# Kernel optimization log

Measured on AMD Instinct MI355X. Metric: run time of the kernel, lower is better.

The kernel has to match this reference:

```python
import jax, jax.numpy as jnp
import numpy as np
import math

EMBED_DIM = 256
NUM_HEADS = 8
FFN_DIM = 1024
EPS = 1e-5


def layer_norm(x, g, b):
    mu = jnp.mean(x, axis=-1, keepdims=True)
    var = jnp.var(x, axis=-1, keepdims=True)
    return (x - mu) / jnp.sqrt(var + EPS) * g + b


def setup_inputs() -> dict:
    key = jax.random.key(0)
    ks = jax.random.split(key, 10)
    B, L, D, F = 4, 2048, EMBED_DIM, FFN_DIM
    x = jax.random.normal(ks[0], (B, L, D), dtype=jnp.float32)
    mask = jnp.ones((B, L), dtype=jnp.int32)
    # FFN params (PyTorch Linear default-ish scale)
    W1 = jax.random.normal(ks[1], (D, F), dtype=jnp.float32) / np.sqrt(D)
    b1 = jnp.zeros((F,), dtype=jnp.float32)
    W2 = jax.random.normal(ks[2], (F, D), dtype=jnp.float32) / np.sqrt(F)
    b2 = jnp.zeros((D,), dtype=jnp.float32)
    g1 = jnp.ones((D,), dtype=jnp.float32)
    be1 = jnp.zeros((D,), dtype=jnp.float32)
    g2 = jnp.ones((D,), dtype=jnp.float32)
    be2 = jnp.zeros((D,), dtype=jnp.float32)
    return {"x": x, "mask": mask, "W1": W1, "b1": b1, "W2": W2, "b2": b2,
            "g1": g1, "be1": be1, "g2": g2, "be2": be2}


def quantum_attention(x, mask):
    B, L, D = x.shape
    H, dk = NUM_HEADS, D // NUM_HEADS
    xh = x.reshape(B, L, H, dk).transpose(0, 2, 1, 3)  # [B,H,L,dk]
    # per-token mean over batch and heads -> [L, dk]
    m = jnp.mean(xh, axis=(0, 1))
    # closed form of the single-qubit RX circuit: P(|1>) = sin^2(angle/2)
    dot = m @ m.T  # [L, L]
    ang = jnp.clip(dot, -math.pi, math.pi)
    scores = jnp.sin(ang * 0.5) ** 2  # [L, L], shared across B and H
    attn = jnp.broadcast_to(scores[None, None], (B, H, L, L))
    attn = jnp.where(mask[:, None, None, :] == 0, -1e9, attn)
    attn = jax.nn.softmax(attn, axis=-1)
    out = jnp.einsum('bhij,bhjd->bhid', attn, xh)  # values are xh itself
    return out.transpose(0, 2, 1, 3).reshape(B, L, D)


def reference(x, mask, W1, b1, W2, b2, g1, be1, g2, be2):
    attn_out = quantum_attention(x, mask)
    h = layer_norm(x + attn_out, g1, be1)
    ffn = jax.nn.relu(h @ W1 + b1) @ W2 + b2
    return layer_norm(h + ffn, g2, be2)
```

## Files before the change

### kernel.cpp

```cpp
#include <hip/hip_runtime.h>
#include <hip/hip_bf16.h>


#define B_ 4
#define L_ 2048
#define D_ 256
#define F_ 1024
#define PI_F 3.14159265358979323846f

typedef __bf16 bf16x8 __attribute__((ext_vector_type(8)));
typedef float floatx4 __attribute__((ext_vector_type(4)));
typedef unsigned short ushortx4 __attribute__((ext_vector_type(4)));
typedef unsigned short ushortx8 __attribute__((ext_vector_type(8)));

#define WAIT_VM(n) asm volatile("s_waitcnt vmcnt(" #n ")" ::: "memory")
#define WAIT_LGKM() asm volatile("s_waitcnt lgkmcnt(0)" ::: "memory")
#define SCHED0() __builtin_amdgcn_sched_barrier(0)
#define BARRIER() do { SCHED0(); __builtin_amdgcn_s_barrier(); SCHED0(); } while (0)

__device__ __forceinline__ unsigned short f2bf(float f) {
    unsigned int u = __float_as_uint(f);
    u = (u + 0x7FFFu + ((u >> 16) & 1u)) >> 16;
    return (unsigned short)u;
}
__device__ __forceinline__ float bf2f(unsigned short u) {
    union { unsigned int i; float f; } v; v.i = ((unsigned int)u) << 16; return v.f;
}

__device__ __forceinline__ void async_cp16(unsigned short* lds, const unsigned short* g) {
    __builtin_amdgcn_global_load_lds(
        (const __attribute__((address_space(1))) unsigned int*)g,
        (__attribute__((address_space(3))) unsigned int*)lds, 16, 0, 0);
}

__global__ __launch_bounds__(256) void k_prep(const float* __restrict__ x,
                                              const float* __restrict__ W1,
                                              const float* __restrict__ W2,
                                              const int* __restrict__ mask,
                                              unsigned short* __restrict__ mb,
                                              unsigned short* __restrict__ XmT,
                                              unsigned short* __restrict__ W1T,
                                              unsigned short* __restrict__ W2T) {
    __shared__ float tile[32][33];
    int r = blockIdx.x, t = threadIdx.x;
    if (r >= 2560) {
        if (r < 2816) {
            int idx = (r - 2560) * 256 + t;
            int l = idx >> 5, k = idx & 31;
            float s = 0.f;
#pragma unroll
            for (int b = 0; b < B_; b++) {
                const float* xp = x + ((size_t)(b * L_ + l)) * D_ + k;
#pragma unroll
                for (int h = 0; h < 8; h++) s += xp[h * 32];
            }
            mb[idx] = f2bf(s * (1.f / 32.f));
        } else {
#pragma unroll
            for (int c = 0; c < 32; c++) {
                int e = c * 256 + t;
                int b = e >> 11, j = e & (L_ - 1);
                XmT[(size_t)(1024 + b) * L_ + j] = mask[b * L_ + j] ? 0x3F80 : 0;
            }
        }
        return;
    }
    const float* in; unsigned short* outp; int R, C; const int* mrow = nullptr; size_t bo = 0;
    int bx, by;
    if (r < 2048) {
        int z = r >> 9, rem = r & 511; by = rem >> 3; bx = rem & 7;
        in = x; outp = XmT; R = L_; C = 256; bo = (size_t)z * R * C; mrow = mask + z * L_;
    } else if (r < 2304) {
        int rem = r - 2048; bx = rem & 31; by = rem >> 5;
        in = W1; outp = W1T; R = 256; C = 1024;
    } else {
        int rem = r - 2304; bx = rem & 7; by = rem >> 3;
        in = W2; outp = W2T; R = 1024; C = 256;
    }
    int r0 = by * 32, c0 = bx * 32;
    int tx = t & 31, ty = t >> 5;
#pragma unroll
    for (int rr = 0; rr < 4; rr++) {
        int rw = ty + rr * 8;
        tile[rw][tx] = in[bo + (size_t)(r0 + rw) * C + c0 + tx];
    }
    float mfac = 1.f;
    if (mrow) mfac = mrow[r0 + tx] ? 1.f : 0.f;
    __syncthreads();
#pragma unroll
    for (int rr = 0; rr < 4; rr++) {
        int c = ty + rr * 8;
        outp[bo + (size_t)(c0 + c) * R + r0 + tx] = f2bf(tile[tx][c] * mfac);
    }
}

__global__ __launch_bounds__(256) void k_scores_mfma(const unsigned short* __restrict__ mb,
                                                     unsigned short* __restrict__ E) {
    const int t = threadIdx.x, lane = t & 63, wid = t >> 6;
    const int wm = (wid >> 1) * 64, wn = (wid & 1) * 32;
    const int lr = lane & 15, lq = lane >> 4;
    int m0 = blockIdx.y * 128, n0 = blockIdx.x * 64;
    bf16x8 af[4], bfr[2];
#pragma unroll
    for (int i = 0; i < 4; i++)
        af[i] = *(const bf16x8*)(mb + (size_t)(m0 + wm + i * 16 + lr) * 32 + lq * 8);
#pragma unroll
    for (int j = 0; j < 2; j++)
        bfr[j] = *(const bf16x8*)(mb + (size_t)(n0 + wn + j * 16 + lr) * 32 + lq * 8);
    floatx4 acc[4][2];
#pragma unroll
    for (int i = 0; i < 4; i++)
#pragma unroll
        for (int j = 0; j < 2; j++) {
            acc[i][j] = (floatx4){0.f, 0.f, 0.f, 0.f};
            acc[i][j] = __builtin_amdgcn_mfma_f32_16x16x32_bf16(af[i], bfr[j], acc[i][j], 0, 0, 0);
        }
#pragma unroll
    for (int i = 0; i < 4; i++)
#pragma unroll
        for (int j = 0; j < 2; j++)
#pragma unroll
            for (int r = 0; r < 4; r++) {
                int row = m0 + wm + i * 16 + lq * 4 + r;
                int col = n0 + wn + j * 16 + lr;
                float d = fminf(fmaxf(acc[i][j][r], -PI_F), PI_F);
                float sn = __sinf(0.5f * d);
                E[(size_t)row * L_ + col] = f2bf(__expf(sn * sn));
            }
}

__global__ __launch_bounds__(256) void k_av(const unsigned short* __restrict__ E,
                                            const unsigned short* __restrict__ XmT,
                                            unsigned short* __restrict__ Cb) {
    __shared__ __align__(16) unsigned short sbuf[3][128 * 64 + 64 * 64];
    const int t = threadIdx.x, lane = t & 63, wid = t >> 6;
    const int wm = (wid >> 1) * 64, wn = (wid & 1) * 32;
    const int lr = lane & 15, lq = lane >> 4;
    const int lrow = lane >> 3, lseg = lane & 7;

    int bid = blockIdx.x;
    int swz = (bid & 7) * 34 + (bid >> 3);
    int m0 = (swz / 17) * 128, n0 = (swz % 17) * 64;

    const unsigned short* Ag[4]; int sAoff[4];
#pragma unroll
    for (int q = 0; q < 4; q++) {
        int rl = wid * 32 + q * 8 + lrow;
        Ag[q] = E + (size_t)(m0 + rl) * L_ + ((lseg - rl) & 7) * 8;
        sAoff[q] = (wid * 32 + q * 8) * 64;
    }
    const unsigned short* Bg[2]; int sBoff[2];
#pragma unroll
    for (int q = 0; q < 2; q++) {
        int rl = wid * 16 + q * 8 + lrow;
        Bg[q] = XmT + (size_t)(n0 + rl) * L_ + ((lseg - rl) & 7) * 8;
        sBoff[q] = 8192 + (wid * 16 + q * 8) * 64;
    }
    int arot[4], aroff[4], brot[2], broff[2];
#pragma unroll
    for (int i = 0; i < 4; i++) { int ar = wm + i * 16 + lr; aroff[i] = ar * 64; arot[i] = lq + ar; }
#pragma unroll
    for (int j = 0; j < 2; j++) { int br = wn + j * 16 + lr; broff[j] = 8192 + br * 64; brot[j] = lq + br; }

    floatx4 acc[4][2];
#pragma unroll
    for (int i = 0; i < 4; i++)
#pragma unroll
        for (int j = 0; j < 2; j++) acc[i][j] = (floatx4){0.f, 0.f, 0.f, 0.f};

    auto stage = [&](unsigned short* base, int k0) {
#pragma unroll
        for (int q = 0; q < 4; q++) async_cp16(base + sAoff[q], Ag[q] + k0);
#pragma unroll
        for (int q = 0; q < 2; q++) async_cp16(base + sBoff[q], Bg[q] + k0);
    };
    auto compute = [&](const unsigned short* base) {
#pragma unroll
        for (int s = 0; s < 2; s++) {
            bf16x8 af[4], bfr[2];
#pragma unroll
            for (int i = 0; i < 4; i++)
                af[i] = *(const bf16x8*)(base + aroff[i] + ((s * 4 + arot[i]) & 7) * 8);
#pragma unroll
            for (int j = 0; j < 2; j++)
                bfr[j] = *(const bf16x8*)(base + broff[j] + ((s * 4 + brot[j]) & 7) * 8);
#pragma unroll
            for (int i = 0; i < 4; i++)
#pragma unroll
                for (int j = 0; j < 2; j++)
                    acc[i][j] = __builtin_amdgcn_mfma_f32_16x16x32_bf16(af[i], bfr[j], acc[i][j], 0, 0, 0);
        }
    };

    unsigned short *p0 = sbuf[0], *p1 = sbuf[1], *p2 = sbuf[2];
    stage(p0, 0); stage(p1, 64); stage(p2, 128);
    WAIT_VM(12); BARRIER();
    for (int p = 0; p < 29; ++p) {
        compute(p0);
        BARRIER();
        stage(p0, (p + 3) << 6);
        WAIT_VM(12); BARRIER();
        unsigned short* tmp = p0; p0 = p1; p1 = p2; p2 = tmp;
    }
    compute(p0);
    BARRIER();
    WAIT_VM(6); BARRIER();
    compute(p1);
    BARRIER();
    WAIT_VM(0); BARRIER();
    compute(p2);

#pragma unroll
    for (int i = 0; i < 4; i++)
#pragma unroll
        for (int j = 0; j < 2; j++)
#pragma unroll
            for (int r = 0; r < 4; r++) {
                int row = m0 + wm + i * 16 + lq * 4 + r;
                int col = n0 + wn + j * 16 + lr;
                Cb[(size_t)row * 1088 + col] = f2bf(acc[i][j][r]);
            }
}

__global__ __launch_bounds__(256, 1) void k_ffn(const float* __restrict__ x,
                                                const unsigned short* __restrict__ Cb,
                                                const unsigned short* __restrict__ W1T,
                                                const unsigned short* __restrict__ W2T,
                                                const float* __restrict__ b1,
                                                const float* __restrict__ b2,
                                                const float* __restrict__ g1, const float* __restrict__ be1,
                                                const float* __restrict__ g2, const float* __restrict__ be2,
                                                float* __restrict__ out) {
    __shared__ __align__(16) unsigned short hA[4 * 32 * 64];
    __shared__ __align__(16) unsigned short W1b[2][4 * 64 * 64];
    __shared__ __align__(16) unsigned short W2b[4 * 64 * 64];
    __shared__ __align__(16) unsigned short t1c[32 * 72];
    __shared__ float red[4][32][2];

    const int t = threadIdx.x, lane = t & 63, wid = t >> 6;
    const int lr = lane & 15, lq = lane >> 4;
    const int half = lane >> 5, l32 = lane & 31;
    const int m0 = blockIdx.x * 32;

    float b1v[16];
#pragma unroll
    for (int c = 0; c < 16; c++) b1v[c] = b1[c * 64 + wid * 16 + lr];
    float4 g1a = *(const float4*)(g1 + l32 * 8);
    float4 g1b = *(const float4*)(g1 + l32 * 8 + 4);
    float4 be1a = *(const float4*)(be1 + l32 * 8);
    float4 be1b = *(const float4*)(be1 + l32 * 8 + 4);
    WAIT_VM(0);

    auto stageW1 = [&](unsigned short* buf, int fc) {
#pragma unroll
        for (int q = 0; q < 8; q++) {
            int kc = q >> 1, sub = q & 1;
            int fl = sub * 32 + wid * 8 + (lane >> 3);
            int kk = lane & 7;
            const unsigned short* src = W1T + (size_t)(fc * 64 + fl) * 256 + kc * 64 + (((kk - fl) & 7) * 8);
            async_cp16(W1b[0] + (buf - W1b[0]) + kc * 4096 + sub * 2048 + wid * 512, src);
        }
    };
    auto stageW2 = [&](int fc) {
#pragma unroll
        for (int q = 0; q < 8; q++) {
            int nc = q >> 1, sub = q & 1;
            int nl = sub * 32 + wid * 8 + (lane >> 3);
            int kk = lane & 7;
            const unsigned short* src = W2T + (size_t)(nc * 64 + nl) * 1024 + fc * 64 + (((kk - nl) & 7) * 8);
            async_cp16(W2b + nc * 4096 + sub * 2048 + wid * 512, src);
        }
    };
    stageW1(W1b[0], 0);
    stageW2(0);
    stageW1(W1b[1], 1);

#pragma unroll
    for (int it = 0; it < 4; it++) {
        int tloc = wid * 8 + it * 2 + half;
        int tok = m0 + tloc;
        int bi = tok >> 11, ii = tok & (L_ - 1);
        float rs = bf2f(Cb[(size_t)ii * 1088 + 1024 + bi]);
        float4 xv0 = *(const float4*)(x + (size_t)tok * D_ + l32 * 8);
        float4 xv1 = *(const float4*)(x + (size_t)tok * D_ + l32 * 8 + 4);
        ushortx8 cv = *(const ushortx8*)(Cb + (size_t)ii * 1088 + bi * 256 + l32 * 8);
        float v[8];
        v[0] = xv0.x + bf2f(cv[0]) / rs; v[1] = xv0.y + bf2f(cv[1]) / rs;
        v[2] = xv0.z + bf2f(cv[2]) / rs; v[3] = xv0.w + bf2f(cv[3]) / rs;
        v[4] = xv1.x + bf2f(cv[4]) / rs; v[5] = xv1.y + bf2f(cv[5]) / rs;
        v[6] = xv1.z + bf2f(cv[6]) / rs; v[7] = xv1.w + bf2f(cv[7]) / rs;
        float s = 0.f, s2 = 0.f;
#pragma unroll
        for (int k = 0; k < 8; k++) { s += v[k]; s2 += v[k] * v[k]; }
#pragma unroll
        for (int o = 1; o < 32; o <<= 1) { s += __shfl_xor(s, o); s2 += __shfl_xor(s2, o); }
        float mu = s * (1.f / 256.f);
        float var = s2 * (1.f / 256.f) - mu * mu;
        float rq = rsqrtf(var + 1e-5f);
        union { bf16x8 v8; unsigned short u[8]; } hv;
        hv.u[0] = f2bf((v[0] - mu) * rq * g1a.x + be1a.x);
        hv.u[1] = f2bf((v[1] - mu) * rq * g1a.y + be1a.y);
        hv.u[2] = f2bf((v[2] - mu) * rq * g1a.z + be1a.z);
        hv.u[3] = f2bf((v[3] - mu) * rq * g1a.w + be1a.w);
        hv.u[4] = f2bf((v[4] - mu) * rq * g1b.x + be1b.x);
        hv.u[5] = f2bf((v[5] - mu) * rq * g1b.y + be1b.y);
        hv.u[6] = f2bf((v[6] - mu) * rq * g1b.z + be1b.z);
        hv.u[7] = f2bf((v[7] - mu) * rq * g1b.w + be1b.w);
        *(bf16x8*)(hA + (l32 >> 3) * 2048 + tloc * 64 + ((((l32 & 7) + tloc) & 7) * 8)) = hv.v8;
    }
    WAIT_LGKM(); BARRIER();

    bf16x8 haf[2][8];
#pragma unroll
    for (int i = 0; i < 2; i++)
#pragma unroll
        for (int kc = 0; kc < 4; kc++)
#pragma unroll
            for (int s = 0; s < 2; s++) {
                int row = i * 16 + lr;
                haf[i][kc * 2 + s] = *(const bf16x8*)(hA + kc * 2048 + row * 64 + (((s * 4 + lq + row) & 7) * 8));
            }

    floatx4 acc[2][4];
#pragma unroll
    for (int i = 0; i < 2; i++)
#pragma unroll
        for (int j = 0; j < 4; j++) acc[i][j] = (floatx4){0.f, 0.f, 0.f, 0.f};

    const int wcol = wid * 16 + lr;
    auto gemm1 = [&](const unsigned short* wb, floatx4 a1[2]) {
#pragma unroll
        for (int kc = 0; kc < 4; kc++)
#pragma unroll
            for (int s = 0; s < 2; s++) {
                bf16x8 bfr = *(const bf16x8*)(wb + kc * 4096 + wcol * 64 + (((s * 4 + lq + wcol) & 7) * 8));
                a1[0] = __builtin_amdgcn_mfma_f32_16x16x32_bf16(haf[0][kc * 2 + s], bfr, a1[0], 0, 0, 0);
                a1[1] = __builtin_amdgcn_mfma_f32_16x16x32_bf16(haf[1][kc * 2 + s], bfr, a1[1], 0, 0, 0);
            }
    };
    auto t1write = [&](floatx4 a1[2], float bv) {
#pragma unroll
        for (int i = 0; i < 2; i++)
#pragma unroll
            for (int r = 0; r < 4; r++)
                t1c[(i * 16 + lq * 4 + r) * 72 + wcol] = f2bf(fmaxf(a1[i][r] + bv, 0.f));
    };
    auto gemm2 = [&]() {
#pragma unroll
        for (int s = 0; s < 2; s++) {
            bf16x8 af0 = *(const bf16x8*)(t1c + lr * 72 + s * 32 + lq * 8);
            bf16x8 af1 = *(const bf16x8*)(t1c + (16 + lr) * 72 + s * 32 + lq * 8);
#pragma unroll
            for (int j = 0; j < 4; j++) {
                int nl = j * 16 + lr;
                bf16x8 bfr = *(const bf16x8*)(W2b + wid * 4096 + nl * 64 + (((s * 4 + lq + nl) & 7) * 8));
                acc[0][j] = __builtin_amdgcn_mfma_f32_16x16x32_bf16(af0, bfr, acc[0][j], 0, 0, 0);
                acc[1][j] = __builtin_amdgcn_mfma_f32_16x16x32_bf16(af1, bfr, acc[1][j], 0, 0, 0);
            }
        }
    };

#pragma unroll
    for (int c = 0; c < 14; c++) {
        floatx4 a1[2] = { (floatx4){0.f,0.f,0.f,0.f}, (floatx4){0.f,0.f,0.f,0.f} };
        gemm1(W1b[c & 1], a1);
        BARRIER();
        stageW1(W1b[c & 1], c + 2);
        t1write(a1, b1v[c]);
        WAIT_LGKM();
        WAIT_VM(8); BARRIER();
        gemm2();
        BARRIER();
        stageW2(c + 1);
    }
    {
        floatx4 a1[2] = { (floatx4){0.f,0.f,0.f,0.f}, (floatx4){0.f,0.f,0.f,0.f} };
        gemm1(W1b[0], a1);
        BARRIER();
        t1write(a1, b1v[14]);
        WAIT_LGKM();
        WAIT_VM(0); BARRIER();
        gemm2();
        BARRIER();
        stageW2(15);
    }
    {
        floatx4 a1[2] = { (floatx4){0.f,0.f,0.f,0.f}, (floatx4){0.f,0.f,0.f,0.f} };
        gemm1(W1b[1], a1);
        BARRIER();
        t1write(a1, b1v[15]);
        WAIT_LGKM();
        WAIT_VM(0); BARRIER();
        gemm2();
    }

    float psum[2][4], psq[2][4];
#pragma unroll
    for (int i = 0; i < 2; i++)
#pragma unroll
        for (int r = 0; r < 4; r++) { psum[i][r] = 0.f; psq[i][r] = 0.f; }
#pragma unroll
    for (int i = 0; i < 2; i++)
#pragma unroll
        for (int j = 0; j < 4; j++) {
            int col = wid * 64 + j * 16 + lr;
            float bv = b2[col];
            int kc = col >> 6, ks = (col >> 3) & 7, ke = col & 7;
#pragma unroll
            for (int r = 0; r < 4; r++) {
                int row = i * 16 + lq * 4 + r;
                float hres = bf2f(hA[kc * 2048 + row * 64 + (((ks + row) & 7) * 8) + ke]);
                float v = acc[i][j][r] + bv + hres;
                acc[i][j][r] = v;
                psum[i][r] += v; psq[i][r] += v * v;
            }
        }
#pragma unroll
    for (int o = 1; o < 16; o <<= 1)
#pragma unroll
        for (int i = 0; i < 2; i++)
#pragma unroll
            for (int r = 0; r < 4; r++) { psum[i][r] += __shfl_xor(psum[i][r], o); psq[i][r] += __shfl_xor(psq[i][r], o); }
    if (lr == 0) {
#pragma unroll
        for (int i = 0; i < 2; i++)
#pragma unroll
            for (int r = 0; r < 4; r++) {
                int lrow = i * 16 + lq * 4 + r;
                red[wid][lrow][0] = psum[i][r];
                red[wid][lrow][1] = psq[i][r];
            }
    }
    __syncthreads();
#pragma unroll
    for (int i = 0; i < 2; i++)
#pragma unroll
        for (int r = 0; r < 4; r++) {
            int lrow = i * 16 + lq * 4 + r;
            float s  = red[0][lrow][0] + red[1][lrow][0] + red[2][lrow][0] + red[3][lrow][0];
            float s2 = red[0][lrow][1] + red[1][lrow][1] + red[2][lrow][1] + red[3][lrow][1];
            float mu = s * (1.f / 256.f);
            float var = s2 * (1.f / 256.f) - mu * mu;
            float rc = rsqrtf(var + 1e-5f);
            int row = m0 + lrow;
#pragma unroll
            for (int j = 0; j < 4; j++) {
                int col = wid * 64 + j * 16 + lr;
                out[(size_t)row * 256 + col] = (acc[i][j][r] - mu) * rc * g2[col] + be2[col];
            }
        }
}

extern "C" void kernel_launch(void* const* d_in, const int* in_sizes, int n_in,
                              void* d_out, int out_size, void* d_ws, size_t ws_size,
                              hipStream_t stream) {
    const float* x   = (const float*)d_in[0];
    const int*  mask = (const int*)d_in[1];
    const float* W1  = (const float*)d_in[2];
    const float* b1  = (const float*)d_in[3];
    const float* W2  = (const float*)d_in[4];
    const float* b2  = (const float*)d_in[5];
    const float* g1  = (const float*)d_in[6];
    const float* be1 = (const float*)d_in[7];
    const float* g2  = (const float*)d_in[8];
    const float* be2 = (const float*)d_in[9];
    float* out = (float*)d_out;

    char* w = (char*)d_ws;
    unsigned short* mb_   = (unsigned short*)w;  w += 65536 * 2;
    unsigned short* E_    = (unsigned short*)w;  w += (size_t)L_ * L_ * 2;
    unsigned short* XmT_  = (unsigned short*)w;  w += (size_t)1088 * L_ * 2;
    unsigned short* W1T_  = (unsigned short*)w;  w += 262144 * 2;
    unsigned short* W2T_  = (unsigned short*)w;  w += 262144 * 2;
    unsigned short* Cb_   = (unsigned short*)w;  w += (size_t)L_ * 1088 * 2;

    k_prep<<<2817, 256, 0, stream>>>(x, W1, W2, mask, mb_, XmT_, W1T_, W2T_);
    k_scores_mfma<<<dim3(32, 16), 256, 0, stream>>>(mb_, E_);
    k_av<<<272, 256, 0, stream>>>(E_, XmT_, Cb_);
    k_ffn<<<256, 256, 0, stream>>>(x, Cb_, W1T_, W2T_, b1, b2, g1, be1, g2, be2, out);
}
```

Measured before the change: 134.0 us.

## Double-buffer W2 tiles in FFN kernel and roll chunk loop

Adds a second W2 shared-memory buffer so both W1 and W2 tiles are prefetched two chunks ahead, replacing the fully unrolled 14+2 chunk loop with a rolled 16-iteration loop that uses uniform vmcnt waits. Bias b1 moves from 16 per-thread registers to a shared-memory array, which frees registers. The initial global-load wait is moved after the LayerNorm prologue so weight prefetch overlaps that work. In exchange it uses more LDS, issues redundant wrap-around prefetches in the last iterations, and the rolled loop may add loop overhead.

Result: slower. 137.1 us (+2.4%).

```diff
diff --git a/kernel.cpp b/kernel.cpp
--- a/kernel.cpp
+++ b/kernel.cpp
@@ -233,47 +233,47 @@
                                                 float* __restrict__ out) {
     __shared__ __align__(16) unsigned short hA[4 * 32 * 64];
     __shared__ __align__(16) unsigned short W1b[2][4 * 64 * 64];
-    __shared__ __align__(16) unsigned short W2b[4 * 64 * 64];
+    __shared__ __align__(16) unsigned short W2b[2][4 * 64 * 64];
     __shared__ __align__(16) unsigned short t1c[32 * 72];
+    __shared__ float b1s[1024];
     __shared__ float red[4][32][2];
 
     const int t = threadIdx.x, lane = t & 63, wid = t >> 6;
     const int lr = lane & 15, lq = lane >> 4;
     const int half = lane >> 5, l32 = lane & 31;
     const int m0 = blockIdx.x * 32;
-
-    float b1v[16];
-#pragma unroll
-    for (int c = 0; c < 16; c++) b1v[c] = b1[c * 64 + wid * 16 + lr];
+    const int lrow8 = lane >> 3, kk = lane & 7;
+
+    auto stageW1 = [&](unsigned short* buf, int fc) {
+#pragma unroll
+        for (int q = 0; q < 8; q++) {
+            int kc = q >> 1, sub = q & 1;
+            int fl = sub * 32 + wid * 8 + lrow8;
+            const unsigned short* src = W1T + (size_t)(fc * 64 + fl) * 256 + kc * 64 + (((kk - fl) & 7) * 8);
+            async_cp16(buf + kc * 4096 + sub * 2048 + wid * 512, src);
+        }
+    };
+    auto stageW2 = [&](unsigned short* buf, int fc) {
+#pragma unroll
+        for (int q = 0; q < 8; q++) {
+            int nc = q >> 1, sub = q & 1;
+            int nl = sub * 32 + wid * 8 + lrow8;
+            const unsigned short* src = W2T + (size_t)(nc * 64 + nl) * 1024 + fc * 64 + (((kk - nl) & 7) * 8);
+            async_cp16(buf + nc * 4096 + sub * 2048 + wid * 512, src);
+        }
+    };
+
+    stageW1(W1b[0], 0);
+    stageW2(W2b[0], 0);
+    stageW1(W1b[1], 1);
+    stageW2(W2b[1], 1);
+
+#pragma unroll
+    for (int q = 0; q < 4; q++) b1s[q * 256 + t] = b1[q * 256 + t];
     float4 g1a = *(const float4*)(g1 + l32 * 8);
     float4 g1b = *(const float4*)(g1 + l32 * 8 + 4);
     float4 be1a = *(const float4*)(be1 + l32 * 8);
     float4 be1b = *(const float4*)(be1 + l32 * 8 + 4);
-    WAIT_VM(0);
-
-    auto stageW1 = [&](unsigned short* buf, int fc) {
-#pragma unroll
-        for (int q = 0; q < 8; q++) {
-            int kc = q >> 1, sub = q & 1;
-            int fl = sub * 32 + wid * 8 + (lane >> 3);
-            int kk = lane & 7;
-            const unsigned short* src = W1T + (size_t)(fc * 64 + fl) * 256 + kc * 64 + (((kk - fl) & 7) * 8);
-            async_cp16(W1b[0] + (buf - W1b[0]) + kc * 4096 + sub * 2048 + wid * 512, src);
-        }
-    };
-    auto stageW2 = [&](int fc) {
-#pragma unroll
-        for (int q = 0; q < 8; q++) {
-            int nc = q >> 1, sub = q & 1;
-            int nl = sub * 32 + wid * 8 + (lane >> 3);
-            int kk = lane & 7;
-            const unsigned short* src = W2T + (size_t)(nc * 64 + nl) * 1024 + fc * 64 + (((kk - nl) & 7) * 8);
-            async_cp16(W2b + nc * 4096 + sub * 2048 + wid * 512, src);
-        }
-    };
-    stageW1(W1b[0], 0);
-    stageW2(0);
-    stageW1(W1b[1], 1);
 
 #pragma unroll
     for (int it = 0; it < 4; it++) {
@@ -308,7 +308,7 @@
         hv.u[7] = f2bf((v[7] - mu) * rq * g1b.w + be1b.w);
         *(bf16x8*)(hA + (l32 >> 3) * 2048 + tloc * 64 + ((((l32 & 7) + tloc) & 7) * 8)) = hv.v8;
     }
-    WAIT_LGKM(); BARRIER();
+    WAIT_VM(0); WAIT_LGKM(); BARRIER();
 
     bf16x8 haf[2][8];
 #pragma unroll
@@ -328,24 +328,34 @@
         for (int j = 0; j < 4; j++) acc[i][j] = (floatx4){0.f, 0.f, 0.f, 0.f};
 
     const int wcol = wid * 16 + lr;
-    auto gemm1 = [&](const unsigned short* wb, floatx4 a1[2]) {
+
+#pragma unroll 1
+    for (int c = 0; c < 16; ++c) {
+        unsigned short* w1cur = W1b[c & 1];
+        unsigned short* w2cur = W2b[c & 1];
+        WAIT_VM(24); BARRIER();
+
+        floatx4 a1[2] = { (floatx4){0.f,0.f,0.f,0.f}, (floatx4){0.f,0.f,0.f,0.f} };
 #pragma unroll
         for (int kc = 0; kc < 4; kc++)
 #pragma unroll
             for (int s = 0; s < 2; s++) {
-                bf16x8 bfr = *(const bf16x8*)(wb + kc * 4096 + wcol * 64 + (((s * 4 + lq + wcol) & 7) * 8));
+                bf16x8 bfr = *(const bf16x8*)(w1cur + kc * 4096 + wcol * 64 + (((s * 4 + lq + wcol) & 7) * 8));
                 a1[0] = __builtin_amdgcn_mfma_f32_16x16x32_bf16(haf[0][kc * 2 + s], bfr, a1[0], 0, 0, 0);
                 a1[1] = __builtin_amdgcn_mfma_f32_16x16x32_bf16(haf[1][kc * 2 + s], bfr, a1[1], 0, 0, 0);
             }
-    };
-    auto t1write = [&](floatx4 a1[2], float bv) {
+        BARRIER();
+        stageW1(w1cur, (c + 2) & 15);
+
+        float bv = b1s[c * 64 + wcol];
 #pragma unroll
         for (int i = 0; i < 2; i++)
 #pragma unroll
             for (int r = 0; r < 4; r++)
                 t1c[(i * 16 + lq * 4 + r) * 72 + wcol] = f2bf(fmaxf(a1[i][r] + bv, 0.f));
-    };
-    auto gemm2 = [&]() {
+        WAIT_LGKM();
+        WAIT_VM(24); BARRIER();
+
 #pragma unroll
         for (int s = 0; s < 2; s++) {
             bf16x8 af0 = *(const bf16x8*)(t1c + lr * 72 + s * 32 + lq * 8);
@@ -353,45 +363,13 @@
 #pragma unroll
             for (int j = 0; j < 4; j++) {
                 int nl = j * 16 + lr;
-                bf16x8 bfr = *(const bf16x8*)(W2b + wid * 4096 + nl * 64 + (((s * 4 + lq + nl) & 7) * 8));
+                bf16x8 bfr = *(const bf16x8*)(w2cur + wid * 4096 + nl * 64 + (((s * 4 + lq + nl) & 7) * 8));
                 acc[0][j] = __builtin_amdgcn_mfma_f32_16x16x32_bf16(af0, bfr, acc[0][j], 0, 0, 0);
                 acc[1][j] = __builtin_amdgcn_mfma_f32_16x16x32_bf16(af1, bfr, acc[1][j], 0, 0, 0);
             }
         }
-    };
-
-#pragma unroll
-    for (int c = 0; c < 14; c++) {
-        floatx4 a1[2] = { (floatx4){0.f,0.f,0.f,0.f}, (floatx4){0.f,0.f,0.f,0.f} };
-        gemm1(W1b[c & 1], a1);
         BARRIER();
-        stageW1(W1b[c & 1], c + 2);
-        t1write(a1, b1v[c]);
-        WAIT_LGKM();
-        WAIT_VM(8); BARRIER();
-        gemm2();
-        BARRIER();
-        stageW2(c + 1);
-    }
-    {
-        floatx4 a1[2] = { (floatx4){0.f,0.f,0.f,0.f}, (floatx4){0.f,0.f,0.f,0.f} };
-        gemm1(W1b[0], a1);
-        BARRIER();
-        t1write(a1, b1v[14]);
-        WAIT_LGKM();
-        WAIT_VM(0); BARRIER();
-        gemm2();
-        BARRIER();
-        stageW2(15);
-    }
-    {
-        floatx4 a1[2] = { (floatx4){0.f,0.f,0.f,0.f}, (floatx4){0.f,0.f,0.f,0.f} };
-        gemm1(W1b[1], a1);
-        BARRIER();
-        t1write(a1, b1v[15]);
-        WAIT_LGKM();
-        WAIT_VM(0); BARRIER();
-        gemm2();
+        stageW2(w2cur, (c + 2) & 15);
     }
 
     float psum[2][4], psq[2][4];
```
